# Kernel tuning notes

Measured on AMD Instinct MI355X. Metric: run time of the kernel, lower is better.

## Reference

```python
import jax, jax.numpy as jnp
import numpy as np


def _hippo_dplr(n):
    # HiPPO-LegS -> NPLR -> DPLR (diagonal plus low rank) init, as in S4
    pr = np.sqrt(1.0 + 2.0 * np.arange(n))
    A = -(np.tril(pr[:, None] * pr[None, :]) - np.diag(np.arange(n)))
    p = np.sqrt(np.arange(n) + 0.5)
    b = np.sqrt(2.0 * np.arange(n) + 1.0)
    S = A + p[:, None] * p[None, :]
    lam_re = np.full(n, np.mean(np.diagonal(S)))
    lam_im, V = np.linalg.eigh(S * -1j)  # S*-1j is Hermitian
    p_c = V.conj().T @ p.astype(np.complex128)
    b_c = V.conj().T @ b.astype(np.complex128)
    return lam_re, lam_im, p_c, b_c


def setup_inputs():
    B, L, H, N = 4, 1024, 512, 64
    key = jax.random.key(0)
    kx, kc, ks, k1, k2 = jax.random.split(key, 5)
    lam_re, lam_im, p_c, b_c = _hippo_dplr(N)
    c = jax.random.normal(kc, (N, 2)) * (0.5 ** 0.5)
    f32 = lambda a: jnp.asarray(a, dtype=jnp.float32)
    return {
        'x': jax.random.normal(kx, (B, L, H), dtype=jnp.float32),
        'norm_weight': jnp.ones((H,), jnp.float32),
        'norm_bias': jnp.zeros((H,), jnp.float32),
        'lambda_re': f32(lam_re), 'lambda_im': f32(lam_im),
        'p_re': f32(p_c.real), 'p_im': f32(p_c.imag),
        'b_re': f32(b_c.real), 'b_im': f32(b_c.imag),
        'c_re': c[:, 0].astype(jnp.float32), 'c_im': c[:, 1].astype(jnp.float32),
        'd': jnp.ones((), jnp.float32),
        'log_step': jax.random.uniform(ks, (), jnp.float32, float(np.log(0.001)), float(np.log(0.1))),
        'out_w': (jax.random.normal(k1, (H, H), jnp.float32) / np.sqrt(H)).astype(jnp.float32),
        'out_b': jnp.zeros((H,), jnp.float32),
        'out2_w': (jax.random.normal(k2, (H, H), jnp.float32) / np.sqrt(H)).astype(jnp.float32),
        'out2_b': jnp.zeros((H,), jnp.float32),
    }


def reference(x, norm_weight, norm_bias, lambda_re, lambda_im, p_re, p_im,
              b_re, b_im, c_re, c_im, d, log_step, out_w, out_b, out2_w, out2_b):
    Bsz, L, H = x.shape
    skip = x
    # LayerNorm over channel dim (eps=1e-5, eqx default)
    mu = jnp.mean(x, -1, keepdims=True)
    var = jnp.mean((x - mu) ** 2, -1, keepdims=True)
    xn = (x - mu) / jnp.sqrt(var + 1e-5) * norm_weight + norm_bias
    # --- S4 DPLR bilinear discretization ---
    lam = (lambda_re + 1j * lambda_im).astype(jnp.complex64)
    p = (p_re + 1j * p_im).astype(jnp.complex64)
    b = (b_re + 1j * b_im).astype(jnp.complex64)
    c = (c_re + 1j * c_im).astype(jnp.complex64)
    step = jnp.exp(log_step).astype(jnp.complex64)
    N = lam.shape[0]
    I = jnp.eye(N, dtype=jnp.complex64)
    A = jnp.diag(lam) - p[:, None] * p[None, :].conj()
    A0 = (2.0 / step) * I + A
    Dinv = jnp.diag(1.0 / ((2.0 / step) - lam))
    qcD = p.conj()[None, :] @ Dinv           # [1,N]
    Dp = Dinv @ p[:, None]                   # [N,1]
    A1 = Dinv - (Dp @ qcD) / (1.0 + (qcD @ p[:, None]))  # Woodbury
    Ab = A1 @ A0                             # [N,N] discrete state matrix
    Bb = 2.0 * (A1 @ b[:, None])[:, 0]       # [N]
    # --- sequential state-space scan over time, vectorized over (B,H) lanes ---
    u = xn.astype(jnp.complex64)             # [B,L,H]

    def step_fn(state, u_t):                 # state: [B,H,N], u_t: [B,H]
        new = jnp.einsum('nm,bhm->bhn', Ab, state) + u_t[..., None] * Bb
        return new, jnp.einsum('n,bhn->bh', c, new).real

    init = jnp.zeros((Bsz, H, N), jnp.complex64)
    _, ys = jax.lax.scan(step_fn, init, jnp.moveaxis(u, 1, 0))  # ys: [L,B,H]
    y = jnp.moveaxis(ys, 0, 1) + d * xn      # feedthrough term
    # --- GELU + GLU-style gated output projection, residual ---
    y = jax.nn.gelu(y)
    gate = jax.nn.sigmoid(y @ out2_w.T + out2_b)
    return skip + (y @ out_w.T + out_b) * gate
```

## Files before the change

### kernel.cpp

```cpp
#include <hip/hip_runtime.h>
#include <math.h>

#define HDIM 512
#define LSEQ 1024
#define BSZ  4

typedef __attribute__((ext_vector_type(8))) short short8;
typedef __attribute__((ext_vector_type(4))) float floatx4;
typedef _Float16 half8 __attribute__((ext_vector_type(8)));

__device__ __forceinline__ float2 cmul(float2 a, float2 b) {
  float2 r;
  r.x = a.x * b.x - a.y * b.y;
  r.y = a.x * b.y + a.y * b.x;
  return r;
}
__device__ __forceinline__ float2 cadd(float2 a, float2 b) {
  float2 r; r.x = a.x + b.x; r.y = a.y + b.y; return r;
}
__device__ __forceinline__ float2 cfma(float2 a, float2 b, float2 c) {
  c.x += a.x * b.x - a.y * b.y;
  c.y += a.x * b.y + a.y * b.x;
  return c;
}
__device__ __forceinline__ ushort f2h(float f) {
  _Float16 h = (_Float16)f;
  return *(ushort*)&h;
}

__global__ __launch_bounds__(576) void stage1_kernel(
    const float* __restrict__ x, const float* __restrict__ nw,
    const float* __restrict__ nb, float* __restrict__ xn,
    const float* __restrict__ lre, const float* __restrict__ lim,
    const float* __restrict__ pre, const float* __restrict__ pim,
    const float* __restrict__ bre, const float* __restrict__ bim,
    const float* __restrict__ cre, const float* __restrict__ cim,
    const float* __restrict__ logstep, float* __restrict__ Kout,
    const float* __restrict__ w1, const float* __restrict__ w2,
    ushort* __restrict__ Wst) {
  __shared__ float2 Ldab[64], Lu[64], Lr[64], LBb[64];
  __shared__ float2 Rv[2048];
  __shared__ float2 Wv[2048];
  int tid = threadIdx.x;
  int wv = tid >> 6;
  int lane = tid & 63;

  if (blockIdx.x != 0) {
    int row = (blockIdx.x - 1) * 9 + wv;
    if (row < BSZ * LSEQ) {
      const float* xr = x + (size_t)row * HDIM;
      float4 v0 = ((const float4*)xr)[lane];
      float4 v1 = ((const float4*)xr)[lane + 64];
      float s  = v0.x + v0.y + v0.z + v0.w + v1.x + v1.y + v1.z + v1.w;
      float ss = v0.x*v0.x + v0.y*v0.y + v0.z*v0.z + v0.w*v0.w
               + v1.x*v1.x + v1.y*v1.y + v1.z*v1.z + v1.w*v1.w;
      #pragma unroll
      for (int m = 1; m < 64; m <<= 1) { s += __shfl_xor(s, m); ss += __shfl_xor(ss, m); }
      float mu   = s * (1.0f / HDIM);
      float var  = ss * (1.0f / HDIM) - mu * mu;
      float rstd = rsqrtf(var + 1e-5f);
      float4 w0 = ((const float4*)nw)[lane];
      float4 w1v = ((const float4*)nw)[lane + 64];
      float4 b0 = ((const float4*)nb)[lane];
      float4 b1 = ((const float4*)nb)[lane + 64];
      float4 o0, o1;
      o0.x = (v0.x - mu) * rstd * w0.x + b0.x;
      o0.y = (v0.y - mu) * rstd * w0.y + b0.y;
      o0.z = (v0.z - mu) * rstd * w0.z + b0.z;
      o0.w = (v0.w - mu) * rstd * w0.w + b0.w;
      o1.x = (v1.x - mu) * rstd * w1v.x + b1.x;
      o1.y = (v1.y - mu) * rstd * w1v.y + b1.y;
      o1.z = (v1.z - mu) * rstd * w1v.z + b1.z;
      o1.w = (v1.w - mu) * rstd * w1v.w + b1.w;
      float* xo = xn + (size_t)row * HDIM;
      ((float4*)xo)[lane] = o0;
      ((float4*)xo)[lane + 64] = o1;
    }
    int idx = (blockIdx.x - 1) * 576 + tid;
    if (idx < 65536) {
      int e0 = idx * 8;
      int n = e0 >> 9, k0 = e0 & 511;
      const float* Wr = (n < 512) ? (w1 + (size_t)n * 512 + k0)
                                  : (w2 + (size_t)(n - 512) * 512 + k0);
      ushort tmp[8];
      #pragma unroll
      for (int q = 0; q < 8; q++) tmp[q] = f2h(Wr[q]);
      *(short8*)&Wst[e0] = *(short8*)tmp;
    }
    return;
  }

  if (tid < 64) {
    int n = tid;
    float step = expf(logstep[0]);
    float g = 2.0f / step;
    float lr = lre[n], li = lim[n];
    float pr = pre[n], pi = pim[n];
    float br = bre[n], bi = bim[n];
    float den  = (g - lr) * (g - lr) + li * li;
    float dinr = (g - lr) / den, dini = li / den;
    float dabr = (g + lr) * dinr - li * dini;
    float dabi = (g + lr) * dini + li * dinr;
    float ur = dinr * pr - dini * pi;
    float ui = dinr * pi + dini * pr;
    float qr = pr * dinr + pi * dini;
    float qi = pr * dini - pi * dinr;
    float pm2 = pr * pr + pi * pi;
    float betr = pm2 * dinr, beti = pm2 * dini;
    float gar = qr * br - qi * bi;
    float gai = qr * bi + qi * br;
    #pragma unroll
    for (int m = 1; m < 64; m <<= 1) {
      betr += __shfl_xor(betr, m); beti += __shfl_xor(beti, m);
      gar  += __shfl_xor(gar, m);  gai  += __shfl_xor(gai, m);
    }
    float obr = 1.0f + betr, obi = beti;
    float ob2 = obr * obr + obi * obi;
    float kr = -2.0f * g * obr / ob2;
    float ki =  2.0f * g * obi / ob2;
    float rr = kr * qr - ki * qi;
    float ri = kr * qi + ki * qr;
    float tgr = (gar * obr + gai * obi) / ob2;
    float tgi = (gai * obr - gar * obi) / ob2;
    float dbr = dinr * br - dini * bi;
    float dbi = dinr * bi + dini * br;
    float Bbr = 2.0f * (dbr - (ur * tgr - ui * tgi));
    float Bbi = 2.0f * (dbi - (ur * tgi + ui * tgr));
    float2 t;
    t.x = dabr; t.y = dabi; Ldab[n] = t;
    t.x = ur;   t.y = ui;   Lu[n]   = t;
    t.x = rr;   t.y = ri;   Lr[n]   = t;
    t.x = Bbr;  t.y = Bbi;  LBb[n]  = t;
  }
  if (wv == 8) { float2 cc; cc.x = cre[lane]; cc.y = cim[lane]; Rv[lane] = cc; }
  __syncthreads();

  int g8 = lane >> 3;
  int q8 = lane & 7;
  int jm = wv * 8 + g8;
  float2 cv[8];

  if (wv < 8) {
    float2 dab[8], u[8], rn[8];
    #pragma unroll
    for (int ii = 0; ii < 8; ii++) {
      int n = q8 * 8 + ii;
      dab[ii] = Ldab[n]; u[ii] = Lu[n]; rn[ii] = Lr[n];
    }
    float2 rj = Lr[jm];
    #pragma unroll
    for (int ii = 0; ii < 8; ii++) {
      int n = q8 * 8 + ii;
      cv[ii] = cmul(u[ii], rj);
      if (n == jm) cv[ii] = cadd(cv[ii], dab[ii]);
    }
    for (int s = 0; s < 31; s++) {
      float2 part; part.x = 0.f; part.y = 0.f;
      #pragma unroll
      for (int ii = 0; ii < 8; ii++) part = cfma(rn[ii], cv[ii], part);
      #pragma unroll
      for (int m = 1; m < 8; m <<= 1) {
        part.x += __shfl_xor(part.x, m);
        part.y += __shfl_xor(part.y, m);
      }
      #pragma unroll
      for (int ii = 0; ii < 8; ii++) {
        float2 nc = cmul(dab[ii], cv[ii]);
        cv[ii] = cfma(u[ii], part, nc);
      }
    }
  } else {
    float2 dab0 = Ldab[lane], u0 = Lu[lane], r0 = Lr[lane];
    float2 w = LBb[lane];
    Wv[lane * 32 + 0] = w;
    for (int b = 1; b < 32; b++) {
      float dr = r0.x * w.x - r0.y * w.y;
      float di = r0.x * w.y + r0.y * w.x;
      #pragma unroll
      for (int m = 1; m < 64; m <<= 1) { dr += __shfl_xor(dr, m); di += __shfl_xor(di, m); }
      float2 nw2;
      nw2.x = dab0.x * w.x - dab0.y * w.y + u0.x * dr - u0.y * di;
      nw2.y = dab0.x * w.y + dab0.y * w.x + u0.x * di + u0.y * dr;
      w = nw2;
      Wv[lane * 32 + b] = w;
    }
  }
  __syncthreads();

  for (int a = 1; a < 32; a++) {
    if (wv < 8) {
      float2 part; part.x = 0.f; part.y = 0.f;
      #pragma unroll
      for (int ii = 0; ii < 8; ii++) {
        float2 Rk = Rv[(a - 1) * 64 + q8 * 8 + ii];
        part = cfma(Rk, cv[ii], part);
      }
      #pragma unroll
      for (int m = 1; m < 8; m <<= 1) {
        part.x += __shfl_xor(part.x, m);
        part.y += __shfl_xor(part.y, m);
      }
      if (q8 == 0) Rv[a * 64 + jm] = part;
    }
    __syncthreads();
  }

  for (int midx = tid; midx < 1024; midx += 576) {
    int a = midx >> 5, b = midx & 31;
    float acc = 0.f;
    for (int n = 0; n < 64; n++) {
      float2 R = Rv[a * 64 + n];
      float2 W = Wv[n * 32 + b];
      acc += R.x * W.x - R.y * W.y;
    }
    Kout[midx] = acc;
  }
}

__global__ __launch_bounds__(256) void prep_kernel(
    const float* __restrict__ xn, const float* __restrict__ K,
    ushort* __restrict__ Uhi, ushort* __restrict__ Thi) {
  __shared__ float tile[64][65];
  int blk = blockIdx.x;
  int tid = threadIdx.x;
  if (blk < 512) {
    int ht = blk & 7, lt = (blk >> 3) & 15, b = blk >> 7;
    #pragma unroll
    for (int q = 0; q < 16; q++) {
      int idx = q * 256 + tid;
      int r = idx >> 6, c = idx & 63;
      tile[r][c] = xn[((size_t)(b * LSEQ + lt * 64 + r)) * HDIM + ht * 64 + c];
    }
    __syncthreads();
    #pragma unroll
    for (int q = 0; q < 16; q++) {
      int idx = q * 256 + tid;
      int r = idx >> 6, c = idx & 63;
      size_t off = ((size_t)(b * HDIM + ht * 64 + r)) * LSEQ + lt * 64 + c;
      Uhi[off] = f2h(tile[c][r]);
    }
  } else {
    int r = blk - 512;
    int t = r * 2 + (tid >> 7);
    int tau0 = (tid & 127) * 8;
    ushort hi[8];
    #pragma unroll
    for (int q = 0; q < 8; q++) {
      int tau = tau0 + q;
      float v = (tau <= t) ? K[t - tau] : 0.f;
      hi[q] = f2h(v);
    }
    *(short8*)&Thi[(size_t)t * 1024 + tau0] = *(short8*)hi;
  }
}

__global__ __launch_bounds__(256) void conv_gemm_kernel(
    const ushort* __restrict__ Thi, const ushort* __restrict__ Uhi,
    const float* __restrict__ xn, const float* __restrict__ dptr,
    ushort* __restrict__ A) {
  __shared__ __attribute__((aligned(16))) ushort sbuf[2 * 9216];
  int tid = threadIdx.x;
  int lane = tid & 63;
  int wv = tid >> 6;
  int wm = wv >> 1, wn = wv & 1;
  int by = blockIdx.y;
  int bm = (by < 8) ? by : 23 - by;
  int bn = blockIdx.x;
  floatx4 acc[2][2] = {};
  int srow = tid >> 2;
  int scol = (tid & 3) * 16;
  int ldst = srow * 72 + scol;
  int fr = lane & 15, fq = (lane >> 4) * 8;
  size_t Toff = (size_t)(bm * 64 + srow) * 1024 + scol;
  size_t Uoff = (size_t)(bn * 64 + srow) * 1024 + scol;
  int KT = bm + 1;
  uint4 t0 = *(const uint4*)&Thi[Toff];
  uint4 t1 = *(const uint4*)&Thi[Toff + 8];
  uint4 u0 = *(const uint4*)&Uhi[Uoff];
  uint4 u1 = *(const uint4*)&Uhi[Uoff + 8];
  *(uint4*)&sbuf[ldst]            = t0;
  *(uint4*)&sbuf[ldst + 8]        = t1;
  *(uint4*)&sbuf[ldst + 4608]     = u0;
  *(uint4*)&sbuf[ldst + 4608 + 8] = u1;
  __syncthreads();
  for (int kt = 0; kt < KT; kt++) {
    const ushort* src = sbuf + (kt & 1) * 9216;
    bool more = (kt + 1 < KT);
    if (more) {
      size_t k1 = (size_t)(kt + 1) * 64;
      t0 = *(const uint4*)&Thi[Toff + k1];
      t1 = *(const uint4*)&Thi[Toff + k1 + 8];
      u0 = *(const uint4*)&Uhi[Uoff + k1];
      u1 = *(const uint4*)&Uhi[Uoff + k1 + 8];
    }
    half8 ah[2][2], bh[2][2];
    #pragma unroll
    for (int i = 0; i < 2; i++) {
      int ar = (wm * 32 + i * 16 + fr) * 72;
      int br = 4608 + (wn * 32 + i * 16 + fr) * 72;
      ah[i][0] = *(const half8*)&src[ar + fq];
      ah[i][1] = *(const half8*)&src[ar + 32 + fq];
      bh[i][0] = *(const half8*)&src[br + fq];
      bh[i][1] = *(const half8*)&src[br + 32 + fq];
    }
    #pragma unroll
    for (int ks = 0; ks < 2; ks++)
      #pragma unroll
      for (int i = 0; i < 2; i++)
        #pragma unroll
        for (int j = 0; j < 2; j++)
          acc[i][j] = __builtin_amdgcn_mfma_f32_16x16x32_f16(ah[i][ks], bh[j][ks], acc[i][j], 0, 0, 0);
    if (more) {
      ushort* dst = sbuf + ((kt & 1) ^ 1) * 9216;
      *(uint4*)&dst[ldst]            = t0;
      *(uint4*)&dst[ldst + 8]        = t1;
      *(uint4*)&dst[ldst + 4608]     = u0;
      *(uint4*)&dst[ldst + 4608 + 8] = u1;
      __syncthreads();
    }
  }
  float d = dptr[0];
  int row0 = bm * 64 + wm * 32;
  int col0 = bn * 64 + wn * 32;
  int fc = lane & 15, frq = (lane >> 4) * 4;
  #pragma unroll
  for (int i = 0; i < 2; i++)
    #pragma unroll
    for (int j = 0; j < 2; j++)
      #pragma unroll
      for (int r = 0; r < 4; r++) {
        int t = row0 + i * 16 + frq + r;
        int c = col0 + j * 16 + fc;
        int b = c >> 9, h = c & 511;
        size_t off = (size_t)(b * LSEQ + t) * HDIM + h;
        float y = acc[i][j][r] + d * xn[off];
        float z2 = 1.5957691216057308f * y * (1.0f + 0.044715f * y * y);
        float sg = __builtin_amdgcn_rcpf(1.0f + __expf(-z2));
        A[off] = f2h(y * sg);
      }
}

__global__ __launch_bounds__(256) void proj_kernel(
    const ushort* __restrict__ Abuf, const ushort* __restrict__ Wst,
    const float* __restrict__ x, const float* __restrict__ ob,
    const float* __restrict__ o2b, float* __restrict__ out) {
  __shared__ __attribute__((aligned(16))) ushort sbuf[2 * 13824];
  int tid = threadIdx.x;
  int lane = tid & 63;
  int wv = tid >> 6;
  int wm = wv >> 1, wn = wv & 1;
  int bm = blockIdx.y, bn = blockIdx.x;
  int srow = tid >> 2;
  int scol = (tid & 3) * 16;
  int ldst = srow * 72 + scol;
  int fr = lane & 15, fq = (lane >> 4) * 8;
  floatx4 acc1[2][2] = {}, acc2[2][2] = {};
  size_t Aoff  = (size_t)(bm * 64 + srow) * 512 + scol;
  size_t W1off = (size_t)(bn * 64 + srow) * 512 + scol;
  size_t W2off = W1off + (size_t)512 * 512;
  uint4 a0 = *(const uint4*)&Abuf[Aoff];
  uint4 a1 = *(const uint4*)&Abuf[Aoff + 8];
  uint4 v0 = *(const uint4*)&Wst[W1off];
  uint4 v1 = *(const uint4*)&Wst[W1off + 8];
  uint4 v2 = *(const uint4*)&Wst[W2off];
  uint4 v3 = *(const uint4*)&Wst[W2off + 8];
  *(uint4*)&sbuf[ldst]            = a0;
  *(uint4*)&sbuf[ldst + 8]        = a1;
  *(uint4*)&sbuf[ldst + 4608]     = v0;
  *(uint4*)&sbuf[ldst + 4608 + 8] = v1;
  *(uint4*)&sbuf[ldst + 9216]     = v2;
  *(uint4*)&sbuf[ldst + 9216 + 8] = v3;
  __syncthreads();
  for (int kt = 0; kt < 8; kt++) {
    const ushort* src = sbuf + (kt & 1) * 13824;
    bool more = (kt + 1 < 8);
    if (more) {
      int k1 = (kt + 1) * 64;
      a0 = *(const uint4*)&Abuf[Aoff + k1];
      a1 = *(const uint4*)&Abuf[Aoff + k1 + 8];
      v0 = *(const uint4*)&Wst[W1off + k1];
      v1 = *(const uint4*)&Wst[W1off + k1 + 8];
      v2 = *(const uint4*)&Wst[W2off + k1];
      v3 = *(const uint4*)&Wst[W2off + k1 + 8];
    }
    half8 af[2][2], b1[2][2], b2[2][2];
    #pragma unroll
    for (int i = 0; i < 2; i++) {
      int ar  = (wm * 32 + i * 16 + fr) * 72;
      int wr1 = 4608 + (wn * 32 + i * 16 + fr) * 72;
      int wr2 = 9216 + (wn * 32 + i * 16 + fr) * 72;
      af[i][0] = *(const half8*)&src[ar + fq];
      af[i][1] = *(const half8*)&src[ar + 32 + fq];
      b1[i][0] = *(const half8*)&src[wr1 + fq];
      b1[i][1] = *(const half8*)&src[wr1 + 32 + fq];
      b2[i][0] = *(const half8*)&src[wr2 + fq];
      b2[i][1] = *(const half8*)&src[wr2 + 32 + fq];
    }
    #pragma unroll
    for (int ks = 0; ks < 2; ks++)
      #pragma unroll
      for (int i = 0; i < 2; i++)
        #pragma unroll
        for (int j = 0; j < 2; j++) {
          acc1[i][j] = __builtin_amdgcn_mfma_f32_16x16x32_f16(af[i][ks], b1[j][ks], acc1[i][j], 0, 0, 0);
          acc2[i][j] = __builtin_amdgcn_mfma_f32_16x16x32_f16(af[i][ks], b2[j][ks], acc2[i][j], 0, 0, 0);
        }
    if (more) {
      ushort* dst = sbuf + ((kt & 1) ^ 1) * 13824;
      *(uint4*)&dst[ldst]            = a0;
      *(uint4*)&dst[ldst + 8]        = a1;
      *(uint4*)&dst[ldst + 4608]     = v0;
      *(uint4*)&dst[ldst + 4608 + 8] = v1;
      *(uint4*)&dst[ldst + 9216]     = v2;
      *(uint4*)&dst[ldst + 9216 + 8] = v3;
      __syncthreads();
    }
  }
  int row0 = bm * 64 + wm * 32;
  int col0 = bn * 64 + wn * 32;
  int fc = lane & 15, frq = (lane >> 4) * 4;
  #pragma unroll
  for (int i = 0; i < 2; i++)
    #pragma unroll
    for (int j = 0; j < 2; j++)
      #pragma unroll
      for (int r = 0; r < 4; r++) {
        int row = row0 + i * 16 + frq + r;
        int col = col0 + j * 16 + fc;
        float c1 = acc1[i][j][r] + ob[col];
        float c2 = acc2[i][j][r] + o2b[col];
        float gate = __builtin_amdgcn_rcpf(1.0f + __expf(-c2));
        size_t off = (size_t)row * HDIM + col;
        out[off] = x[off] + c1 * gate;
      }
}

extern "C" void kernel_launch(void* const* d_in, const int* in_sizes, int n_in,
                              void* d_out, int out_size, void* d_ws, size_t ws_size,
                              hipStream_t stream) {
  const float* x   = (const float*)d_in[0];
  const float* nw  = (const float*)d_in[1];
  const float* nb  = (const float*)d_in[2];
  const float* lre = (const float*)d_in[3];
  const float* lim = (const float*)d_in[4];
  const float* pre = (const float*)d_in[5];
  const float* pim = (const float*)d_in[6];
  const float* bre = (const float*)d_in[7];
  const float* bim = (const float*)d_in[8];
  const float* cre = (const float*)d_in[9];
  const float* cim = (const float*)d_in[10];
  const float* dsc = (const float*)d_in[11];
  const float* lst = (const float*)d_in[12];
  const float* w1  = (const float*)d_in[13];
  const float* ob  = (const float*)d_in[14];
  const float* w2  = (const float*)d_in[15];
  const float* o2b = (const float*)d_in[16];

  char* ws = (char*)d_ws;
  float* xn    = (float*)(ws);
  ushort* Uhi  = (ushort*)(ws + (size_t)(8  << 20));
  ushort* Thi  = (ushort*)(ws + (size_t)(12 << 20));
  ushort* Wst  = (ushort*)(ws + (size_t)(16 << 20));
  ushort* Abuf = (ushort*)(ws + (size_t)(17 << 20));
  float* Kbuf  = (float*)(ws + (size_t)(21 << 20));
  float* out   = (float*)d_out;

  stage1_kernel<<<dim3(457), dim3(576), 0, stream>>>(x, nw, nb, xn,
                                                     lre, lim, pre, pim, bre, bim,
                                                     cre, cim, lst, Kbuf,
                                                     w1, w2, Wst);
  prep_kernel<<<dim3(1024), dim3(256), 0, stream>>>(xn, Kbuf, Uhi, Thi);
  conv_gemm_kernel<<<dim3(32, 16), dim3(256), 0, stream>>>(Thi, Uhi,
                                                           xn, dsc, Abuf);
  proj_kernel<<<dim3(8, 64), dim3(256), 0, stream>>>(Abuf, Wst, x, ob, o2b, out);
}
```

Baseline: 151.1 us.

## Store layernormed activations in fp16 and vectorize transpose, skip unused Toeplitz blocks

The layernorm output is now written as fp16 instead of fp32, which halves the traffic for the intermediate that prep and conv_gemm read. The transpose in prep_kernel now uses 16-byte vector loads and stores through an fp16 shared tile. The Toeplitz fill also skips tau blocks beyond the causal tile boundary, since the GEMM only reads up to bm+1 K-tiles. The cost is that the feedthrough term d*xn now reads an fp16-rounded value, which adds a small precision loss.

```diff
diff --git a/kernel.cpp b/kernel.cpp
--- a/kernel.cpp
+++ b/kernel.cpp
@@ -27,10 +27,13 @@
   _Float16 h = (_Float16)f;
   return *(ushort*)&h;
 }
+__device__ __forceinline__ uint pack2h(float a, float b) {
+  return (uint)f2h(a) | ((uint)f2h(b) << 16);
+}
 
 __global__ __launch_bounds__(576) void stage1_kernel(
     const float* __restrict__ x, const float* __restrict__ nw,
-    const float* __restrict__ nb, float* __restrict__ xn,
+    const float* __restrict__ nb, ushort* __restrict__ xn16,
     const float* __restrict__ lre, const float* __restrict__ lim,
     const float* __restrict__ pre, const float* __restrict__ pim,
     const float* __restrict__ bre, const float* __restrict__ bim,
@@ -72,9 +75,12 @@
       o1.y = (v1.y - mu) * rstd * w1v.y + b1.y;
       o1.z = (v1.z - mu) * rstd * w1v.z + b1.z;
       o1.w = (v1.w - mu) * rstd * w1v.w + b1.w;
-      float* xo = xn + (size_t)row * HDIM;
-      ((float4*)xo)[lane] = o0;
-      ((float4*)xo)[lane + 64] = o1;
+      ushort* xo = xn16 + (size_t)row * HDIM;
+      uint2 p0, p1;
+      p0.x = pack2h(o0.x, o0.y); p0.y = pack2h(o0.z, o0.w);
+      p1.x = pack2h(o1.x, o1.y); p1.y = pack2h(o1.z, o1.w);
+      *(uint2*)&xo[lane * 4]       = p0;
+      *(uint2*)&xo[256 + lane * 4] = p1;
     }
     int idx = (blockIdx.x - 1) * 576 + tid;
     if (idx < 65536) {
@@ -218,45 +224,50 @@
 }
 
 __global__ __launch_bounds__(256) void prep_kernel(
-    const float* __restrict__ xn, const float* __restrict__ K,
+    const ushort* __restrict__ xn16, const float* __restrict__ K,
     ushort* __restrict__ Uhi, ushort* __restrict__ Thi) {
-  __shared__ float tile[64][65];
+  __shared__ __attribute__((aligned(16))) ushort tile[64][72];
   int blk = blockIdx.x;
   int tid = threadIdx.x;
   if (blk < 512) {
     int ht = blk & 7, lt = (blk >> 3) & 15, b = blk >> 7;
-    #pragma unroll
-    for (int q = 0; q < 16; q++) {
-      int idx = q * 256 + tid;
-      int r = idx >> 6, c = idx & 63;
-      tile[r][c] = xn[((size_t)(b * LSEQ + lt * 64 + r)) * HDIM + ht * 64 + c];
-    }
+    int r = tid >> 2;
+    int sc = (tid & 3) * 16;
+    const ushort* src = xn16 + ((size_t)(b * LSEQ + lt * 64 + r)) * HDIM + ht * 64 + sc;
+    uint4 va = *(const uint4*)&src[0];
+    uint4 vb = *(const uint4*)&src[8];
+    *(uint4*)&tile[r][sc]     = va;
+    *(uint4*)&tile[r][sc + 8] = vb;
     __syncthreads();
-    #pragma unroll
-    for (int q = 0; q < 16; q++) {
-      int idx = q * 256 + tid;
-      int r = idx >> 6, c = idx & 63;
-      size_t off = ((size_t)(b * HDIM + ht * 64 + r)) * LSEQ + lt * 64 + c;
-      Uhi[off] = f2h(tile[c][r]);
-    }
+    int hr = tid >> 2;
+    int c0 = (tid & 3) * 16;
+    ushort tmp[16];
+    #pragma unroll
+    for (int q = 0; q < 16; q++) tmp[q] = tile[c0 + q][hr];
+    ushort* dst = Uhi + ((size_t)(b * HDIM + ht * 64 + hr)) * LSEQ + lt * 64 + c0;
+    *(uint4*)&dst[0] = *(uint4*)&tmp[0];
+    *(uint4*)&dst[8] = *(uint4*)&tmp[8];
   } else {
     int r = blk - 512;
     int t = r * 2 + (tid >> 7);
     int tau0 = (tid & 127) * 8;
-    ushort hi[8];
-    #pragma unroll
-    for (int q = 0; q < 8; q++) {
-      int tau = tau0 + q;
-      float v = (tau <= t) ? K[t - tau] : 0.f;
-      hi[q] = f2h(v);
-    }
-    *(short8*)&Thi[(size_t)t * 1024 + tau0] = *(short8*)hi;
+    int bound = ((t >> 6) + 1) << 6;
+    if (tau0 < bound) {
+      ushort hi[8];
+      #pragma unroll
+      for (int q = 0; q < 8; q++) {
+        int tau = tau0 + q;
+        float v = (tau <= t) ? K[t - tau] : 0.f;
+        hi[q] = f2h(v);
+      }
+      *(short8*)&Thi[(size_t)t * 1024 + tau0] = *(short8*)hi;
+    }
   }
 }
 
 __global__ __launch_bounds__(256) void conv_gemm_kernel(
     const ushort* __restrict__ Thi, const ushort* __restrict__ Uhi,
-    const float* __restrict__ xn, const float* __restrict__ dptr,
+    const ushort* __restrict__ xn16, const float* __restrict__ dptr,
     ushort* __restrict__ A) {
   __shared__ __attribute__((aligned(16))) ushort sbuf[2 * 9216];
   int tid = threadIdx.x;
@@ -333,7 +344,8 @@
         int c = col0 + j * 16 + fc;
         int b = c >> 9, h = c & 511;
         size_t off = (size_t)(b * LSEQ + t) * HDIM + h;
-        float y = acc[i][j][r] + d * xn[off];
+        float xv = (float)(*(const _Float16*)&xn16[off]);
+        float y = acc[i][j][r] + d * xv;
         float z2 = 1.5957691216057308f * y * (1.0f + 0.044715f * y * y);
         float sg = __builtin_amdgcn_rcpf(1.0f + __expf(-z2));
         A[off] = f2h(y * sg);
@@ -457,7 +469,7 @@
   const float* o2b = (const float*)d_in[16];
 
   char* ws = (char*)d_ws;
-  float* xn    = (float*)(ws);
+  ushort* xn16 = (ushort*)(ws);
   ushort* Uhi  = (ushort*)(ws + (size_t)(8  << 20));
   ushort* Thi  = (ushort*)(ws + (size_t)(12 << 20));
   ushort* Wst  = (ushort*)(ws + (size_t)(16 << 20));
@@ -465,12 +477,12 @@
   float* Kbuf  = (float*)(ws + (size_t)(21 << 20));
   float* out   = (float*)d_out;
 
-  stage1_kernel<<<dim3(457), dim3(576), 0, stream>>>(x, nw, nb, xn,
+  stage1_kernel<<<dim3(457), dim3(576), 0, stream>>>(x, nw, nb, xn16,
                                                      lre, lim, pre, pim, bre, bim,
                                                      cre, cim, lst, Kbuf,
                                                      w1, w2, Wst);
-  prep_kernel<<<dim3(1024), dim3(256), 0, stream>>>(xn, Kbuf, Uhi, Thi);
+  prep_kernel<<<dim3(1024), dim3(256), 0, stream>>>(xn16, Kbuf, Uhi, Thi);
   conv_gemm_kernel<<<dim3(32, 16), dim3(256), 0, stream>>>(Thi, Uhi,
-                                                           xn, dsc, Abuf);
+                                                           xn16, dsc, Abuf);
   proj_kernel<<<dim3(8, 64), dim3(256), 0, stream>>>(Abuf, Wst, x, ob, o2b, out);
 }
```

After: 151.9 us. Within noise of the previous version (+0.5%).
